# Kernel optimization log

Hardware: AMD Instinct MI355X
Metric: run time of the kernel (lower is better)

The kernel has to match this reference:

```python
import jax, jax.numpy as jnp
import numpy as np

N_NODES = 100000
N_EDGES = 1600000
IN_C, HID_C, OUT_C = 256, 128, 64


def sage_conv(x, src, dst, Wl, Wr, b, n_nodes):
    """PyG SAGEConv: lin_l(mean of neighbor messages) + lin_r(x) + b."""
    msgs = x[src]  # [E, C] gather
    agg = jax.ops.segment_sum(msgs, dst, num_segments=n_nodes)  # [N, C] scatter-add
    deg = jax.ops.segment_sum(jnp.ones((src.shape[0],), x.dtype), dst, num_segments=n_nodes)
    agg = agg / jnp.maximum(deg, 1.0)[:, None]  # mean aggregation, safe for isolated nodes
    return agg @ Wl + x @ Wr + b


def setup_inputs() -> dict:
    key = jax.random.key(0)
    ks = jax.random.split(key, 12)

    def glorot(k, shape):
        fan_in, fan_out = shape
        lim = float(np.sqrt(6.0 / (fan_in + fan_out)))
        return jax.random.uniform(k, shape, jnp.float32, -lim, lim)

    x = jax.random.normal(ks[0], (N_NODES, IN_C), jnp.float32)
    edge_index = jax.random.randint(ks[1], (2, N_EDGES), 0, N_NODES, jnp.int32)
    return {
        "x": x,
        "edge_index": edge_index,
        "Wl0": glorot(ks[2], (IN_C, HID_C)),
        "Wr0": glorot(ks[3], (IN_C, HID_C)),
        "b0": jnp.zeros((HID_C,), jnp.float32),
        "Wl1": glorot(ks[4], (HID_C, HID_C)),
        "Wr1": glorot(ks[5], (HID_C, HID_C)),
        "b1": jnp.zeros((HID_C,), jnp.float32),
        "Wl2": glorot(ks[6], (HID_C, OUT_C)),
        "Wr2": glorot(ks[7], (HID_C, OUT_C)),
        "b2": jnp.zeros((OUT_C,), jnp.float32),
    }


def reference(x, edge_index, Wl0, Wr0, b0, Wl1, Wr1, b1, Wl2, Wr2, b2):
    src, dst = edge_index[0], edge_index[1]
    n = x.shape[0]
    h = x
    out = None
    # convs[:-1]: conv -> relu -> dropout (eval mode: dropout = identity)
    for Wl, Wr, b in ((Wl0, Wr0, b0), (Wl1, Wr1, b1)):
        out = sage_conv(h, src, dst, Wl, Wr, b, n)
        h = jax.nn.relu(out)
    g = h
    x_final = sage_conv(g, src, dst, Wl2, Wr2, b2, n)
    return (x_final, out, g)
```

## Files before the change

kernel.cpp:

```cpp
#include <hip/hip_runtime.h>
#include <stdint.h>

typedef __attribute__((ext_vector_type(4))) float f32x4;
typedef _Float16 half8 __attribute__((ext_vector_type(8)));
typedef _Float16 half4 __attribute__((ext_vector_type(4)));


#define BIN_CHUNK 8192
#define MAXB 512

__global__ __launch_bounds__(256) void k_bhist(const int* __restrict__ dst,
                                               int* __restrict__ bcnt, int E) {
    __shared__ int lh[MAXB];
    for (int i = threadIdx.x; i < MAXB; i += 256) lh[i] = 0;
    __syncthreads();
    const int base = blockIdx.x * BIN_CHUNK;
#pragma unroll 4
    for (int i = 0; i < BIN_CHUNK / 256; i++) {
        int e = base + i * 256 + threadIdx.x;
        if (e < E) atomicAdd(&lh[dst[e] >> 8], 1);
    }
    __syncthreads();
    for (int i = threadIdx.x; i < MAXB; i += 256)
        if (lh[i]) atomicAdd(&bcnt[i], lh[i]);
}

__global__ __launch_bounds__(512) void k_pscan(const int* __restrict__ in,
                                               int* __restrict__ out0,
                                               int* __restrict__ out1,
                                               int* __restrict__ tot, int n) {
    __shared__ int sh[512];
    const int t = threadIdx.x;
    int v[4];
    int s = 0;
#pragma unroll
    for (int i = 0; i < 4; i++) {
        int idx = t * 4 + i;
        v[i] = (idx < n) ? in[idx] : 0;
        s += v[i];
    }
    sh[t] = s;
    __syncthreads();
    for (int off = 1; off < 512; off <<= 1) {
        int add = (t >= off) ? sh[t - off] : 0;
        __syncthreads();
        sh[t] += add;
        __syncthreads();
    }
    int excl = sh[t] - s;
#pragma unroll
    for (int i = 0; i < 4; i++) {
        int idx = t * 4 + i;
        if (idx < n) {
            out0[idx] = excl;
            if (out1) out1[idx] = excl;
        }
        excl += v[i];
    }
    if (t == 511 && tot) *tot = sh[511];
}

__global__ __launch_bounds__(256) void k_bin(const int* __restrict__ src,
                                             const int* __restrict__ dst,
                                             int* __restrict__ gcur,
                                             unsigned* __restrict__ ebuf, int E) {
    __shared__ int lh[MAXB];
    __shared__ int lcur[MAXB];
    for (int i = threadIdx.x; i < MAXB; i += 256) lh[i] = 0;
    __syncthreads();
    const int base = blockIdx.x * BIN_CHUNK;
#pragma unroll 4
    for (int i = 0; i < BIN_CHUNK / 256; i++) {
        int e = base + i * 256 + threadIdx.x;
        if (e < E) atomicAdd(&lh[dst[e] >> 8], 1);
    }
    __syncthreads();
    for (int i = threadIdx.x; i < MAXB; i += 256)
        lcur[i] = lh[i] ? atomicAdd(&gcur[i], lh[i]) : 0;
    __syncthreads();
#pragma unroll 4
    for (int i = 0; i < BIN_CHUNK / 256; i++) {
        int e = base + i * 256 + threadIdx.x;
        if (e < E) {
            int d = dst[e];
            int pos = atomicAdd(&lcur[d >> 8], 1);
            ebuf[pos] = (unsigned)src[e] | ((unsigned)(d & 255) << 24);
        }
    }
}

__global__ __launch_bounds__(256) void k_nhist(const unsigned* __restrict__ ebuf,
                                               const int* __restrict__ bbase,
                                               int* __restrict__ deg, int N) {
    __shared__ int cnt[256];
    cnt[threadIdx.x] = 0;
    __syncthreads();
    const int b = blockIdx.x;
    const int lo = bbase[b], hi = bbase[b + 1];
    for (int e = lo + threadIdx.x; e < hi; e += 256)
        atomicAdd(&cnt[ebuf[e] >> 24], 1);
    __syncthreads();
    int n = (b << 8) + threadIdx.x;
    if (n < N) deg[n] = cnt[threadIdx.x];
}

__global__ __launch_bounds__(256) void k_bfill(const unsigned* __restrict__ ebuf,
                                               const int* __restrict__ bbase,
                                               const int* __restrict__ rowptr,
                                               int* __restrict__ ssrc, int N) {
    __shared__ int lc[256];
    const int b = blockIdx.x;
    int n = (b << 8) + threadIdx.x;
    lc[threadIdx.x] = (n < N) ? rowptr[n] : 0;
    __syncthreads();
    const int lo = bbase[b], hi = bbase[b + 1];
    for (int e = lo + threadIdx.x; e < hi; e += 256) {
        unsigned v = ebuf[e];
        int pos = atomicAdd(&lc[v >> 24], 1);
        ssrc[pos] = (int)(v & 0xFFFFFFu);
    }
}


__global__ void k_scan1(int* __restrict__ buf, int* __restrict__ chunkSum, int N) {
    const int t = threadIdx.x;
    const int base = blockIdx.x * 2048 + t * 8;
    int v[8];
    int s = 0;
#pragma unroll
    for (int i = 0; i < 8; i++) {
        int idx = base + i;
        v[i] = (idx < N) ? buf[idx] : 0;
        s += v[i];
    }
    __shared__ int sh[256];
    sh[t] = s;
    __syncthreads();
    for (int off = 1; off < 256; off <<= 1) {
        int add = (t >= off) ? sh[t - off] : 0;
        __syncthreads();
        sh[t] += add;
        __syncthreads();
    }
    int excl = sh[t] - s;
    int run = excl;
#pragma unroll
    for (int i = 0; i < 8; i++) {
        int idx = base + i;
        if (idx < N) buf[idx] = run;
        run += v[i];
    }
    if (t == 255) chunkSum[blockIdx.x] = sh[255];
}

__global__ void k_scan3(int* __restrict__ rowptr, const int* __restrict__ chunkOff, int N) {
    int i = blockIdx.x * 256 + threadIdx.x;
    if (i < N) rowptr[i] += chunkOff[i >> 11];
}


template <int K, int NCOLT>
__device__ inline void wprep_one(const float* __restrict__ Wl, const float* __restrict__ Wr,
                                 _Float16* __restrict__ Wt, int i) {
    constexpr int NCOL = NCOLT / 2;
    int n = i / K, k = i - n * K;
    float v = (n < NCOL) ? Wl[(size_t)k * NCOL + n] : Wr[(size_t)k * NCOL + (n - NCOL)];
    Wt[(size_t)(k >> 5) * (NCOLT * 32) + n * 32 + (k & 31)] = (_Float16)v;
}

__global__ __launch_bounds__(256) void k_wprepAll(
    const float* __restrict__ Wl0, const float* __restrict__ Wr0,
    const float* __restrict__ Wl1, const float* __restrict__ Wr1,
    const float* __restrict__ Wl2, const float* __restrict__ Wr2,
    _Float16* __restrict__ Wt0, _Float16* __restrict__ Wt1, _Float16* __restrict__ Wt2) {
    int i = blockIdx.x * 256 + threadIdx.x;
    if (i < 65536) wprep_one<256, 256>(Wl0, Wr0, Wt0, i);
    else if (i < 98304) wprep_one<128, 256>(Wl1, Wr1, Wt1, i - 65536);
    else if (i < 114688) wprep_one<128, 128>(Wl2, Wr2, Wt2, i - 98304);
}


template <int K, int NCOLT, bool AF32>
__global__ __launch_bounds__(256) void k_gemmM(const void* __restrict__ Av,
                                               const _Float16* __restrict__ Wt,
                                               const float* __restrict__ bias,
                                               _Float16* __restrict__ Cl,
                                               _Float16* __restrict__ Cr, int M) {
    constexpr int NCOL = NCOLT / 2;
    constexpr int WC = NCOLT / 4;
    constexpr int NT = WC / 16;
    constexpr int AS = K + 8;
    constexpr int CS = NCOLT + 8;
    constexpr int MAXS = (K > NCOLT ? K : NCOLT) + 8;
    __shared__ _Float16 sh[64 * MAXS];

    const int tid = threadIdx.x;
    const int lane = tid & 63;
    const int wave = tid >> 6;
    const int quad = lane >> 4;
    const int l16 = lane & 15;
    const int m0 = blockIdx.x * 64;
    const int colbase = wave * WC;

    if (AF32) {
        const float* A = (const float*)Av;
#pragma unroll
        for (int i = 0; i < K / 16; i++) {
            int off = i * 1024 + tid * 4;
            int row = off / K, col = off % K;
            f32x4 u = {0.f, 0.f, 0.f, 0.f};
            if (m0 + row < M) u = *(const f32x4*)(A + (size_t)(m0 + row) * K + col);
            half4 h = {(_Float16)u[0], (_Float16)u[1], (_Float16)u[2], (_Float16)u[3]};
            *(half4*)(sh + row * AS + col) = h;
        }
    } else {
        const _Float16* A = (const _Float16*)Av;
#pragma unroll
        for (int i = 0; i < K / 32; i++) {
            int off = i * 2048 + tid * 8;
            int row = off / K, col = off % K;
            half8 u = {0, 0, 0, 0, 0, 0, 0, 0};
            if (m0 + row < M) u = *(const half8*)(A + (size_t)(m0 + row) * K + col);
            *(half8*)(sh + row * AS + col) = u;
        }
    }
    __syncthreads();

    f32x4 acc[4][NT];
#pragma unroll
    for (int rg = 0; rg < 4; rg++)
#pragma unroll
        for (int t = 0; t < NT; t++) acc[rg][t] = (f32x4){0.f, 0.f, 0.f, 0.f};

#pragma unroll
    for (int k0 = 0; k0 < K; k0 += 32) {
        half8 a[4];
#pragma unroll
        for (int rg = 0; rg < 4; rg++)
            a[rg] = *(const half8*)(sh + (rg * 16 + l16) * AS + k0 + quad * 8);
        half8 b[NT];
        const _Float16* Wk = Wt + (size_t)(k0 >> 5) * (NCOLT * 32);
#pragma unroll
        for (int t = 0; t < NT; t++)
            b[t] = *(const half8*)(Wk + (colbase + t * 16 + l16) * 32 + quad * 8);
#pragma unroll
        for (int rg = 0; rg < 4; rg++)
#pragma unroll
            for (int t = 0; t < NT; t++)
                acc[rg][t] = __builtin_amdgcn_mfma_f32_16x16x32_f16(b[t], a[rg], acc[rg][t], 0, 0, 0);
    }

    __syncthreads();

#pragma unroll
    for (int t = 0; t < NT; t++) {
        int c0 = colbase + t * 16 + quad * 4;
        f32x4 bv = {0.f, 0.f, 0.f, 0.f};
        if (c0 >= NCOL) bv = *(const f32x4*)(bias + (c0 - NCOL));
#pragma unroll
        for (int rg = 0; rg < 4; rg++) {
            half4 h = {(_Float16)(acc[rg][t][0] + bv[0]), (_Float16)(acc[rg][t][1] + bv[1]),
                       (_Float16)(acc[rg][t][2] + bv[2]), (_Float16)(acc[rg][t][3] + bv[3])};
            *(half4*)(sh + (rg * 16 + l16) * CS + c0) = h;
        }
    }
    __syncthreads();

#pragma unroll
    for (int i = 0; i < (64 * NCOL) / 2048; i++) {
        int off = i * 2048 + tid * 8;
        int row = off / NCOL, col = off % NCOL;
        if (m0 + row < M) {
            *(half8*)(Cl + (size_t)(m0 + row) * NCOL + col) = *(const half8*)(sh + row * CS + col);
            *(half8*)(Cr + (size_t)(m0 + row) * NCOL + col) = *(const half8*)(sh + row * CS + NCOL + col);
        }
    }
}


template <int COUT, int MODE>
__global__ __launch_bounds__(256) void k_agg(const half8* __restrict__ xl,
                                             const half8* __restrict__ xr,
                                             const int* __restrict__ rowptr,
                                             const int* __restrict__ ssrc,
                                             float* __restrict__ outF1,
                                             float* __restrict__ outF2,
                                             _Float16* __restrict__ outH, int N) {
    constexpr int LPN = COUT / 16;
    constexpr int NPB = 256 / LPN;
    constexpr int C8 = COUT / 8;
    const int tid = threadIdx.x;
    const int c = tid % LPN;
    const int n = blockIdx.x * NPB + tid / LPN;
    if (n >= N) return;

    const int rp0 = rowptr[n];
    const int rp1 = rowptr[n + 1];
    float acc[16];
#pragma unroll
    for (int i = 0; i < 16; i++) acc[i] = 0.f;

    const size_t cb = (size_t)c * 2;
    int e = rp0;
    for (; e + 3 < rp1; e += 4) {
        int s0 = ssrc[e], s1 = ssrc[e + 1], s2 = ssrc[e + 2], s3 = ssrc[e + 3];
        half8 v0a = xl[(size_t)s0 * C8 + cb], v0b = xl[(size_t)s0 * C8 + cb + 1];
        half8 v1a = xl[(size_t)s1 * C8 + cb], v1b = xl[(size_t)s1 * C8 + cb + 1];
        half8 v2a = xl[(size_t)s2 * C8 + cb], v2b = xl[(size_t)s2 * C8 + cb + 1];
        half8 v3a = xl[(size_t)s3 * C8 + cb], v3b = xl[(size_t)s3 * C8 + cb + 1];
#pragma unroll
        for (int i = 0; i < 8; i++) {
            acc[i] += (float)v0a[i] + (float)v1a[i] + (float)v2a[i] + (float)v3a[i];
            acc[8 + i] += (float)v0b[i] + (float)v1b[i] + (float)v2b[i] + (float)v3b[i];
        }
    }
    for (; e < rp1; e++) {
        int s = ssrc[e];
        half8 va = xl[(size_t)s * C8 + cb], vb = xl[(size_t)s * C8 + cb + 1];
#pragma unroll
        for (int i = 0; i < 8; i++) {
            acc[i] += (float)va[i];
            acc[8 + i] += (float)vb[i];
        }
    }

    const int deg = rp1 - rp0;
    const float scale = 1.0f / (float)(deg > 1 ? deg : 1);
    half8 x0 = xr[(size_t)n * C8 + cb];
    half8 x1 = xr[(size_t)n * C8 + cb + 1];
    float res[16];
#pragma unroll
    for (int i = 0; i < 8; i++) {
        res[i] = acc[i] * scale + (float)x0[i];
        res[8 + i] = acc[8 + i] * scale + (float)x1[i];
    }

    const size_t ob = (size_t)n * COUT + (size_t)c * 16;
    if (MODE == 0) {
        half8 h0v, h1v;
#pragma unroll
        for (int i = 0; i < 8; i++) {
            h0v[i] = (_Float16)(res[i] > 0.f ? res[i] : 0.f);
            h1v[i] = (_Float16)(res[8 + i] > 0.f ? res[8 + i] : 0.f);
        }
        *(half8*)(outH + ob) = h0v;
        *(half8*)(outH + ob + 8) = h1v;
    } else if (MODE == 1) {
#pragma unroll
        for (int q = 0; q < 4; q++) {
            f32x4 v = {res[q * 4], res[q * 4 + 1], res[q * 4 + 2], res[q * 4 + 3]};
            *(f32x4*)(outF1 + ob + q * 4) = v;
            f32x4 z = {v[0] > 0.f ? v[0] : 0.f, v[1] > 0.f ? v[1] : 0.f,
                       v[2] > 0.f ? v[2] : 0.f, v[3] > 0.f ? v[3] : 0.f};
            *(f32x4*)(outF2 + ob + q * 4) = z;
        }
        half8 h0v, h1v;
#pragma unroll
        for (int i = 0; i < 8; i++) {
            h0v[i] = (_Float16)(res[i] > 0.f ? res[i] : 0.f);
            h1v[i] = (_Float16)(res[8 + i] > 0.f ? res[8 + i] : 0.f);
        }
        *(half8*)(outH + ob) = h0v;
        *(half8*)(outH + ob + 8) = h1v;
    } else {
#pragma unroll
        for (int q = 0; q < 4; q++) {
            f32x4 v = {res[q * 4], res[q * 4 + 1], res[q * 4 + 2], res[q * 4 + 3]};
            *(f32x4*)(outF1 + ob + q * 4) = v;
        }
    }
}


extern "C" void kernel_launch(void* const* d_in, const int* in_sizes, int n_in,
                              void* d_out, int out_size, void* d_ws, size_t ws_size,
                              hipStream_t stream) {
    const float* x   = (const float*)d_in[0];
    const int*   ei  = (const int*)d_in[1];
    const float* Wl0 = (const float*)d_in[2];
    const float* Wr0 = (const float*)d_in[3];
    const float* b0  = (const float*)d_in[4];
    const float* Wl1 = (const float*)d_in[5];
    const float* Wr1 = (const float*)d_in[6];
    const float* b1  = (const float*)d_in[7];
    const float* Wl2 = (const float*)d_in[8];
    const float* Wr2 = (const float*)d_in[9];
    const float* b2  = (const float*)d_in[10];

    const int N = in_sizes[0] / 256;
    const int E = in_sizes[1] / 2;
    const int* src = ei;
    const int* dst = ei + E;

    char* p = (char*)d_ws;
    auto alloc = [&](size_t bytes) -> void* {
        void* r = (void*)p;
        p += (bytes + 255) & ~(size_t)255;
        return r;
    };
    int*      rowptr   = (int*)alloc((size_t)(N + 1) * 4);
    int*      chunkSum = (int*)alloc(64 * 4);
    int*      chunkOff = (int*)alloc(64 * 4);
    int*      bcnt     = (int*)alloc(MAXB * 4);
    int*      bbase    = (int*)alloc((MAXB + 1) * 4);
    int*      gcur     = (int*)alloc(MAXB * 4);
    int*      ssrc     = (int*)alloc((size_t)E * 4);
    _Float16* xl       = (_Float16*)alloc((size_t)N * 128 * 2);
    _Float16* xr       = (_Float16*)alloc((size_t)N * 128 * 2);
    _Float16* h0       = (_Float16*)alloc((size_t)N * 128 * 2);
    _Float16* gb       = (_Float16*)alloc((size_t)N * 128 * 2);
    _Float16* Wt0      = (_Float16*)alloc((size_t)256 * 256 * 2);
    _Float16* Wt1      = (_Float16*)alloc((size_t)256 * 128 * 2);
    _Float16* Wt2      = (_Float16*)alloc((size_t)128 * 128 * 2);

    unsigned* ebuf = (unsigned*)gb;

    float* out = (float*)d_out;
    float* x_final = out;
    float* out1    = out + (size_t)N * 64;
    float* g       = out + (size_t)N * 192;

    const int nb = (N + 255) >> 8;
    const int nbk = (E + BIN_CHUNK - 1) / BIN_CHUNK;
    const int nch = (N + 2047) / 2048;

    hipMemsetAsync(bcnt, 0, MAXB * 4, stream);
    k_bhist<<<nbk, 256, 0, stream>>>(dst, bcnt, E);
    k_pscan<<<1, 512, 0, stream>>>(bcnt, bbase, gcur, bbase + nb, nb);
    k_bin<<<nbk, 256, 0, stream>>>(src, dst, gcur, ebuf, E);
    k_nhist<<<nb, 256, 0, stream>>>(ebuf, bbase, rowptr, N);
    k_scan1<<<nch, 256, 0, stream>>>(rowptr, chunkSum, N);
    k_pscan<<<1, 512, 0, stream>>>(chunkSum, chunkOff, nullptr, rowptr + N, nch);
    k_scan3<<<(N + 255) / 256, 256, 0, stream>>>(rowptr, chunkOff, N);
    k_bfill<<<nb, 256, 0, stream>>>(ebuf, bbase, rowptr, ssrc, N);

    k_wprepAll<<<448, 256, 0, stream>>>(Wl0, Wr0, Wl1, Wr1, Wl2, Wr2, Wt0, Wt1, Wt2);

    const int gGrid = (N + 63) / 64;

    k_gemmM<256, 256, true><<<gGrid, 256, 0, stream>>>(x, Wt0, b0, xl, xr, N);
    k_agg<128, 0><<<(N + 31) / 32, 256, 0, stream>>>((const half8*)xl, (const half8*)xr,
                                                     rowptr, ssrc, nullptr, nullptr, h0, N);

    k_gemmM<128, 256, false><<<gGrid, 256, 0, stream>>>(h0, Wt1, b1, xl, xr, N);
    k_agg<128, 1><<<(N + 31) / 32, 256, 0, stream>>>((const half8*)xl, (const half8*)xr,
                                                     rowptr, ssrc, out1, g, gb, N);

    k_gemmM<128, 128, false><<<gGrid, 256, 0, stream>>>(gb, Wt2, b2, xl, xr, N);
    k_agg<64, 2><<<(N + 63) / 64, 256, 0, stream>>>((const half8*)xl, (const half8*)xr,
                                                    rowptr, ssrc, x_final, nullptr, nullptr, N);
}
```

Measured before the change: 553.2 us.

## Fuse CSR node histogram, scan and fill into one per-bucket kernel

Replaces the five kernels that built the CSR (node histogram, two-level scan, offset add, fill) with a single per-bucket kernel. It counts node degrees in shared memory, does a local block scan offset by the bucket base, writes rowptr and scatters sources. This removes four launches and several global round trips over rowptr. It also adds an 8-edge unrolled gather loop in the aggregation kernel to keep more loads in flight, at the cost of extra registers.

```diff
diff --git a/kernel.cpp b/kernel.cpp
--- a/kernel.cpp
+++ b/kernel.cpp
@@ -89,52 +89,23 @@
     }
 }
 
-__global__ __launch_bounds__(256) void k_nhist(const unsigned* __restrict__ ebuf,
-                                               const int* __restrict__ bbase,
-                                               int* __restrict__ deg, int N) {
+__global__ __launch_bounds__(256) void k_csr(const unsigned* __restrict__ ebuf,
+                                             const int* __restrict__ bbase,
+                                             int* __restrict__ rowptr,
+                                             int* __restrict__ ssrc, int N) {
     __shared__ int cnt[256];
-    cnt[threadIdx.x] = 0;
-    __syncthreads();
+    __shared__ int sh[256];
+    __shared__ int lc[256];
+    const int t = threadIdx.x;
     const int b = blockIdx.x;
+    cnt[t] = 0;
+    __syncthreads();
     const int lo = bbase[b], hi = bbase[b + 1];
-    for (int e = lo + threadIdx.x; e < hi; e += 256)
+    for (int e = lo + t; e < hi; e += 256)
         atomicAdd(&cnt[ebuf[e] >> 24], 1);
     __syncthreads();
-    int n = (b << 8) + threadIdx.x;
-    if (n < N) deg[n] = cnt[threadIdx.x];
-}
-
-__global__ __launch_bounds__(256) void k_bfill(const unsigned* __restrict__ ebuf,
-                                               const int* __restrict__ bbase,
-                                               const int* __restrict__ rowptr,
-                                               int* __restrict__ ssrc, int N) {
-    __shared__ int lc[256];
-    const int b = blockIdx.x;
-    int n = (b << 8) + threadIdx.x;
-    lc[threadIdx.x] = (n < N) ? rowptr[n] : 0;
-    __syncthreads();
-    const int lo = bbase[b], hi = bbase[b + 1];
-    for (int e = lo + threadIdx.x; e < hi; e += 256) {
-        unsigned v = ebuf[e];
-        int pos = atomicAdd(&lc[v >> 24], 1);
-        ssrc[pos] = (int)(v & 0xFFFFFFu);
-    }
-}
-
-
-__global__ void k_scan1(int* __restrict__ buf, int* __restrict__ chunkSum, int N) {
-    const int t = threadIdx.x;
-    const int base = blockIdx.x * 2048 + t * 8;
-    int v[8];
-    int s = 0;
-#pragma unroll
-    for (int i = 0; i < 8; i++) {
-        int idx = base + i;
-        v[i] = (idx < N) ? buf[idx] : 0;
-        s += v[i];
-    }
-    __shared__ int sh[256];
-    sh[t] = s;
+    const int myc = cnt[t];
+    sh[t] = myc;
     __syncthreads();
     for (int off = 1; off < 256; off <<= 1) {
         int add = (t >= off) ? sh[t - off] : 0;
@@ -142,20 +113,16 @@
         sh[t] += add;
         __syncthreads();
     }
-    int excl = sh[t] - s;
-    int run = excl;
-#pragma unroll
-    for (int i = 0; i < 8; i++) {
-        int idx = base + i;
-        if (idx < N) buf[idx] = run;
-        run += v[i];
-    }
-    if (t == 255) chunkSum[blockIdx.x] = sh[255];
-}
-
-__global__ void k_scan3(int* __restrict__ rowptr, const int* __restrict__ chunkOff, int N) {
-    int i = blockIdx.x * 256 + threadIdx.x;
-    if (i < N) rowptr[i] += chunkOff[i >> 11];
+    const int base = lo + (sh[t] - myc);
+    const int n = (b << 8) + t;
+    if (n <= N) rowptr[n] = base;
+    lc[t] = base;
+    __syncthreads();
+    for (int e = lo + t; e < hi; e += 256) {
+        unsigned v = ebuf[e];
+        int pos = atomicAdd(&lc[v >> 24], 1);
+        ssrc[pos] = (int)(v & 0xFFFFFFu);
+    }
 }
 
 
@@ -302,6 +269,25 @@
 
     const size_t cb = (size_t)c * 2;
     int e = rp0;
+    for (; e + 7 < rp1; e += 8) {
+        int s[8];
+#pragma unroll
+        for (int u = 0; u < 8; u++) s[u] = ssrc[e + u];
+        half8 va[8], vb[8];
+#pragma unroll
+        for (int u = 0; u < 8; u++) {
+            const half8* p = xl + (size_t)s[u] * C8 + cb;
+            va[u] = p[0];
+            vb[u] = p[1];
+        }
+#pragma unroll
+        for (int u = 0; u < 8; u++)
+#pragma unroll
+            for (int i = 0; i < 8; i++) {
+                acc[i] += (float)va[u][i];
+                acc[8 + i] += (float)vb[u][i];
+            }
+    }
     for (; e + 3 < rp1; e += 4) {
         int s0 = ssrc[e], s1 = ssrc[e + 1], s2 = ssrc[e + 2], s3 = ssrc[e + 3];
         half8 v0a = xl[(size_t)s0 * C8 + cb], v0b = xl[(size_t)s0 * C8 + cb + 1];
@@ -399,8 +385,6 @@
         return r;
     };
     int*      rowptr   = (int*)alloc((size_t)(N + 1) * 4);
-    int*      chunkSum = (int*)alloc(64 * 4);
-    int*      chunkOff = (int*)alloc(64 * 4);
     int*      bcnt     = (int*)alloc(MAXB * 4);
     int*      bbase    = (int*)alloc((MAXB + 1) * 4);
     int*      gcur     = (int*)alloc(MAXB * 4);
@@ -422,17 +406,12 @@
 
     const int nb = (N + 255) >> 8;
     const int nbk = (E + BIN_CHUNK - 1) / BIN_CHUNK;
-    const int nch = (N + 2047) / 2048;
 
     hipMemsetAsync(bcnt, 0, MAXB * 4, stream);
     k_bhist<<<nbk, 256, 0, stream>>>(dst, bcnt, E);
     k_pscan<<<1, 512, 0, stream>>>(bcnt, bbase, gcur, bbase + nb, nb);
     k_bin<<<nbk, 256, 0, stream>>>(src, dst, gcur, ebuf, E);
-    k_nhist<<<nb, 256, 0, stream>>>(ebuf, bbase, rowptr, N);
-    k_scan1<<<nch, 256, 0, stream>>>(rowptr, chunkSum, N);
-    k_pscan<<<1, 512, 0, stream>>>(chunkSum, chunkOff, nullptr, rowptr + N, nch);
-    k_scan3<<<(N + 255) / 256, 256, 0, stream>>>(rowptr, chunkOff, N);
-    k_bfill<<<nb, 256, 0, stream>>>(ebuf, bbase, rowptr, ssrc, N);
+    k_csr<<<nb, 256, 0, stream>>>(ebuf, bbase, rowptr, ssrc, N);
 
     k_wprepAll<<<448, 256, 0, stream>>>(Wl0, Wr0, Wl1, Wr1, Wl2, Wr2, Wt0, Wt1, Wt2);
 
```

After: 536.5 us. 3.0% less time.
